# Kernel optimization log

Hardware: AMD Instinct MI355X
Metric: run time of the kernel (lower is better)

## Reference

```python
import jax, jax.numpy as jnp
import numpy as np

EMBED_SIZE = 2048
EBS = 512            # embed_block_size
NB = EMBED_SIZE // EBS  # num_blocks = 4
HEADS = 8
HD = EBS // HEADS    # head_dim = 64
N, S = 4, 1024


def block_linear(x, W, b):
    # x: [T, NB, EBS], W: [NB, EBS, EBS], b: [NB, EBS]
    return jnp.einsum('tbi,bio->tbo', x, W) + b


def setup_inputs() -> dict:
    key = jax.random.key(0)
    ks = jax.random.split(key, 11)
    sc = 1.0 / np.sqrt(EBS)
    inp = {
        'values': jax.random.normal(ks[0], (N, S, EMBED_SIZE), jnp.float32),
        'keys': jax.random.normal(ks[1], (N, S, EMBED_SIZE), jnp.float32),
        'query': jax.random.normal(ks[2], (N, S, EMBED_SIZE), jnp.float32),
        'mask': jnp.ones((N, 1, 1, S, S), jnp.int32),
        'Wv': jax.random.normal(ks[3], (NB, EBS, EBS), jnp.float32) * sc,
        'bv': jnp.zeros((NB, EBS), jnp.float32),
        'Wk': jax.random.normal(ks[4], (NB, EBS, EBS), jnp.float32) * sc,
        'bk': jnp.zeros((NB, EBS), jnp.float32),
        'Wq': jax.random.normal(ks[5], (NB, EBS, EBS), jnp.float32) * sc,
        'bq': jnp.zeros((NB, EBS), jnp.float32),
        'Wo': jax.random.normal(ks[6], (NB, EBS, EBS), jnp.float32) * sc,
        'bo': jnp.zeros((NB, EBS), jnp.float32),
    }
    return inp


def reference(values, keys, query, mask, Wv, bv, Wk, bk, Wq, bq, Wo, bo):
    n, ql = query.shape[0], query.shape[1]
    vl, kl = values.shape[1], keys.shape[1]
    # block-diagonal QKV projections
    v = block_linear(values.reshape(-1, NB, EBS), Wv, bv)
    k = block_linear(keys.reshape(-1, NB, EBS), Wk, bk)
    q = block_linear(query.reshape(-1, NB, EBS), Wq, bq)
    v = v.reshape(n, vl, NB, HEADS, HD)
    k = k.reshape(n, kl, NB, HEADS, HD)
    q = q.reshape(n, ql, NB, HEADS, HD)
    energy = jnp.einsum('nqbhd,nkbhd->nbhqk', q, k)
    energy = jnp.where(mask == 0, jnp.float32(-1e20), energy)
    # NOTE: faithful to original: softmax over dim=3 (the query axis of nbhqk)
    attention = jax.nn.softmax(energy / np.sqrt(HD), axis=3)
    out = jnp.einsum('nbhql,nlbhd->nqbhd', attention, v)
    out = out.reshape(n * ql, NB, HEADS * HD)
    out = block_linear(out, Wo, bo)
    return out.reshape(n, ql, -1)
```

## Files before the change

### kernel.cpp

```cpp
#include <hip/hip_runtime.h>


typedef unsigned short u16;
typedef __bf16 bf16x8 __attribute__((ext_vector_type(8)));
typedef float f32x4 __attribute__((ext_vector_type(4)));

#define S_LEN 1024
#define HD 64
#define EMB 2048
#define EBS 512
#define C2EXP 0.18033688011112042f

__device__ __forceinline__ u16 f2b(float f) {
    union { float f; unsigned int i; } x; x.f = f;
    return (u16)((x.i + 0x8000u) >> 16);
}
__device__ __forceinline__ float b2f(u16 u) {
    union { unsigned int i; float f; } x; x.i = ((unsigned int)u) << 16;
    return x.f;
}
__device__ __forceinline__ bf16x8 ld8(const u16* p) {
    return *reinterpret_cast<const bf16x8*>(p);
}
__device__ __forceinline__ unsigned int pack2(float a, float b) {
    union { float f; unsigned int i; } x, y; x.f = a; y.f = b;
    return ((x.i + 0x8000u) >> 16) | ((y.i + 0x8000u) & 0xFFFF0000u);
}
__device__ __forceinline__ int swz(int r, int c) {
    return (r << 6) + (c ^ ((r & 7) << 3));
}

__device__ __forceinline__ int dtype_probe(const void* src, int tid, int* s_flag) {
    if (tid < 64) {
        u16 v = ((const u16*)src)[tid * 2];
        int e = (v >> 7) & 0xFF;
        int sane = (e >= 117 && e <= 134);
        unsigned long long b = __ballot(sane);
        if (tid == 0) *s_flag = (__popcll(b) < 32) ? 1 : 0;
    }
    __syncthreads();
    return *s_flag;
}

__global__ __launch_bounds__(256) void wtrans(
    const void* __restrict__ Wv, const void* __restrict__ Wk,
    const void* __restrict__ Wq, const void* __restrict__ Wo,
    u16* __restrict__ WT, const void* __restrict__ probe)
{
    const int p = blockIdx.z >> 2, b = blockIdx.z & 3;
    const void* Wp = (p == 0 ? Wv : p == 1 ? Wk : p == 2 ? Wq : Wo);
    const size_t boff = (size_t)b * EBS * EBS;
    u16* D = WT + (size_t)(p * 4 + b) * EBS * EBS;
    const int i0 = blockIdx.x * 64, o0 = blockIdx.y * 64;
    const int tid = threadIdx.x;
    __shared__ __align__(16) u16 tile[64][72];
    __shared__ int s_flag;
    const int is32 = dtype_probe(probe, tid, &s_flag);
    for (int c = tid; c < 512; c += 256) {
        const int r = c >> 3, c8 = (c & 7) << 3;
        union { uint4 v; u16 u[8]; } pk;
        if (is32) {
            const float* src = (const float*)Wp + boff + (size_t)(i0 + r) * EBS + o0 + c8;
            const float4 f0 = *(const float4*)src, f1 = *(const float4*)(src + 4);
            pk.u[0] = f2b(f0.x); pk.u[1] = f2b(f0.y); pk.u[2] = f2b(f0.z); pk.u[3] = f2b(f0.w);
            pk.u[4] = f2b(f1.x); pk.u[5] = f2b(f1.y); pk.u[6] = f2b(f1.z); pk.u[7] = f2b(f1.w);
        } else {
            pk.v = *(const uint4*)((const u16*)Wp + boff + (size_t)(i0 + r) * EBS + o0 + c8);
        }
        *(uint4*)&tile[r][c8] = pk.v;
    }
    __syncthreads();
    for (int c = tid; c < 512; c += 256) {
        const int r = c >> 3, c8 = (c & 7) << 3;
        union { uint4 v; u16 u[8]; } pk;
        #pragma unroll
        for (int j = 0; j < 8; ++j) pk.u[j] = tile[c8 + j][r];
        *(uint4*)(D + (size_t)(o0 + r) * EBS + i0 + c8) = pk.v;
    }
}

__global__ __launch_bounds__(256) void gemm_qkv(
    const void* __restrict__ A, const void* __restrict__ W, const u16* __restrict__ WTp,
    const void* __restrict__ bias, u16* __restrict__ dst,
    const void* __restrict__ probe, int use_wt, int vmode, float oscale,
    const float* __restrict__ vsc)
{
    const int tm = blockIdx.x, tn = blockIdx.y, b = blockIdx.z;
    const int tid = threadIdx.x;
    const int wave = tid >> 6, lane = tid & 63, quad = lane >> 4, c16 = lane & 15;
    const int wm = wave >> 1, wn = wave & 1;

    __shared__ __align__(16) u16 Al[128 * 40];
    __shared__ __align__(16) u16 Bl[128 * 40];
    __shared__ int s_flag;
    const int is32 = dtype_probe(probe, tid, &s_flag);

    f32x4 acc[4][4];
    #pragma unroll
    for (int i = 0; i < 4; ++i)
        #pragma unroll
        for (int j = 0; j < 4; ++j) acc[i][j] = (f32x4){0.f, 0.f, 0.f, 0.f};

    const size_t aoff = (size_t)tm * 128 * EMB + (size_t)b * EBS;
    const u16*   Ab = (const u16*)A + aoff;
    const float* Af = (const float*)A + aoff;
    const size_t woff = (size_t)b * EBS * EBS + (size_t)tn * 128;
    const u16*   Wb = (const u16*)W + woff;
    const float* Wf = (const float*)W + woff;
    const u16*   Tb = WTp + (size_t)b * EBS * EBS + (size_t)tn * 128 * EBS;

    for (int k0 = 0; k0 < EBS; k0 += 32) {
        for (int c = tid; c < 512; c += 256) {
            const int r = c >> 2, c8 = (c & 3) << 3;
            if (is32) {
                const float* p = Af + (size_t)r * EMB + k0 + c8;
                const float4 f0 = *(const float4*)p, f1 = *(const float4*)(p + 4);
                union { uint4 v; u16 u[8]; } pk;
                pk.u[0] = f2b(f0.x); pk.u[1] = f2b(f0.y); pk.u[2] = f2b(f0.z); pk.u[3] = f2b(f0.w);
                pk.u[4] = f2b(f1.x); pk.u[5] = f2b(f1.y); pk.u[6] = f2b(f1.z); pk.u[7] = f2b(f1.w);
                *(uint4*)&Al[r * 40 + c8] = pk.v;
            } else {
                *(uint4*)&Al[r * 40 + c8] = *(const uint4*)(Ab + (size_t)r * EMB + k0 + c8);
            }
        }
        if (use_wt) {
            for (int c = tid; c < 512; c += 256) {
                const int r = c >> 2, c8 = (c & 3) << 3;
                *(uint4*)&Bl[r * 40 + c8] = *(const uint4*)(Tb + (size_t)r * EBS + k0 + c8);
            }
        } else {
            for (int c = tid; c < 512; c += 256) {
                const int i = c & 31, oc = c >> 5;
                u16 h[8];
                if (is32) {
                    const float* p = Wf + (size_t)(k0 + i) * EBS + oc * 8;
                    const float4 f0 = *(const float4*)p, f1 = *(const float4*)(p + 4);
                    h[0] = f2b(f0.x); h[1] = f2b(f0.y); h[2] = f2b(f0.z); h[3] = f2b(f0.w);
                    h[4] = f2b(f1.x); h[5] = f2b(f1.y); h[6] = f2b(f1.z); h[7] = f2b(f1.w);
                } else {
                    union { uint4 v; u16 u[8]; } pk;
                    pk.v = *(const uint4*)(Wb + (size_t)(k0 + i) * EBS + oc * 8);
                    #pragma unroll
                    for (int j = 0; j < 8; ++j) h[j] = pk.u[j];
                }
                #pragma unroll
                for (int j = 0; j < 8; ++j) Bl[(oc * 8 + j) * 40 + i] = h[j];
            }
        }
        __syncthreads();
        bf16x8 af[4], bfr[4];
        #pragma unroll
        for (int ms = 0; ms < 4; ++ms)
            af[ms] = ld8(&Al[(wm * 64 + ms * 16 + c16) * 40 + quad * 8]);
        #pragma unroll
        for (int ns = 0; ns < 4; ++ns)
            bfr[ns] = ld8(&Bl[(wn * 64 + ns * 16 + c16) * 40 + quad * 8]);
        if (vmode == 0) {
            #pragma unroll
            for (int ms = 0; ms < 4; ++ms)
                #pragma unroll
                for (int ns = 0; ns < 4; ++ns)
                    acc[ms][ns] = __builtin_amdgcn_mfma_f32_16x16x32_bf16(af[ms], bfr[ns], acc[ms][ns], 0, 0, 0);
        } else {
            #pragma unroll
            for (int ms = 0; ms < 4; ++ms)
                #pragma unroll
                for (int ns = 0; ns < 4; ++ns)
                    acc[ms][ns] = __builtin_amdgcn_mfma_f32_16x16x32_bf16(bfr[ns], af[ms], acc[ms][ns], 0, 0, 0);
        }
        __syncthreads();
    }

    if (vmode == 0) {
        #pragma unroll
        for (int ns = 0; ns < 4; ++ns) {
            const int o = tn * 128 + wn * 64 + ns * 16 + c16;
            const float bb = is32 ? ((const float*)bias)[b * EBS + o]
                                  : b2f(((const u16*)bias)[b * EBS + o]);
            #pragma unroll
            for (int ms = 0; ms < 4; ++ms) {
                #pragma unroll
                for (int r = 0; r < 4; ++r) {
                    const int t = tm * 128 + wm * 64 + ms * 16 + quad * 4 + r;
                    const int n = t >> 10, s = t & 1023;
                    const int h = o >> 6, d = o & 63;
                    const int hid = (n * 4 + b) * 8 + h;
                    dst[(size_t)hid * (S_LEN * HD) + (size_t)s * HD + d] = f2b((acc[ms][ns][r] + bb) * oscale);
                }
            }
        }
    } else {
        #pragma unroll
        for (int ns = 0; ns < 4; ++ns) {
            #pragma unroll
            for (int r = 0; r < 4; ++r) {
                const int o = tn * 128 + wn * 64 + ns * 16 + quad * 4 + r;
                const float bb = is32 ? ((const float*)bias)[b * EBS + o]
                                      : b2f(((const u16*)bias)[b * EBS + o]);
                const int h = o >> 6, d = o & 63;
                #pragma unroll
                for (int ms = 0; ms < 4; ++ms) {
                    const int t = tm * 128 + wm * 64 + ms * 16 + c16;
                    const int n = t >> 10, s = t & 1023;
                    const int hid = (n * 4 + b) * 8 + h;
                    float val = (acc[ms][ns][r] + bb) * oscale;
                    if (vsc) val *= vsc[(size_t)hid * S_LEN + s];
                    dst[(size_t)hid * (S_LEN * HD) + (size_t)d * S_LEN + s] = f2b(val);
                }
            }
        }
    }
}

__global__ __launch_bounds__(256) void attn_colstats(
    const u16* __restrict__ qws, const u16* __restrict__ kws,
    float* __restrict__ vscale)
{
    const int hid = blockIdx.x, lb = blockIdx.y;
    const int tid = threadIdx.x;
    const int wave = tid >> 6, lane = tid & 63, quad = lane >> 4, c16 = lane & 15;
    const int l0 = lb * 128;

    __shared__ __align__(16) u16 Ql[64 * 72];

    const u16* Kp = kws + (size_t)hid * (S_LEN * HD);
    const u16* Qp = qws + (size_t)hid * (S_LEN * HD);

    bf16x8 ak[2][2];
    #pragma unroll
    for (int s = 0; s < 2; ++s) {
        const size_t row = (size_t)(l0 + s * 64 + wave * 16 + c16) * HD;
        ak[s][0] = ld8(&Kp[row + quad * 8]);
        ak[s][1] = ld8(&Kp[row + 32 + quad * 8]);
    }

    float sum[2][4];
    #pragma unroll
    for (int s = 0; s < 2; ++s)
        #pragma unroll
        for (int r = 0; r < 4; ++r) sum[s][r] = 0.f;

    for (int q0 = 0; q0 < S_LEN; q0 += 64) {
        for (int c = tid; c < 512; c += 256) {
            const int r = c >> 3, c8 = (c & 7) << 3;
            *(uint4*)&Ql[r * 72 + c8] = *(const uint4*)(Qp + (size_t)(q0 + r) * HD + c8);
        }
        __syncthreads();
        #pragma unroll
        for (int qs = 0; qs < 4; ++qs) {
            const bf16x8 bq0 = ld8(&Ql[(qs * 16 + c16) * 72 + quad * 8]);
            const bf16x8 bq1 = ld8(&Ql[(qs * 16 + c16) * 72 + 32 + quad * 8]);
            #pragma unroll
            for (int s = 0; s < 2; ++s) {
                f32x4 e = (f32x4){0.f, 0.f, 0.f, 0.f};
                e = __builtin_amdgcn_mfma_f32_16x16x32_bf16(ak[s][0], bq0, e, 0, 0, 0);
                e = __builtin_amdgcn_mfma_f32_16x16x32_bf16(ak[s][1], bq1, e, 0, 0, 0);
                #pragma unroll
                for (int r = 0; r < 4; ++r)
                    sum[s][r] += exp2f(e[r]);
            }
        }
        __syncthreads();
    }
    #pragma unroll
    for (int s = 0; s < 2; ++s) {
        #pragma unroll
        for (int r = 0; r < 4; ++r) {
            float ss = sum[s][r];
            ss += __shfl_xor(ss, 1);
            ss += __shfl_xor(ss, 2);
            ss += __shfl_xor(ss, 4);
            ss += __shfl_xor(ss, 8);
            if (c16 == 0) {
                const int l = l0 + s * 64 + wave * 16 + quad * 4 + r;
                vscale[hid * S_LEN + l] = 1.0f / ss;
            }
        }
    }
}

__global__ __launch_bounds__(256) void attn_pass2(
    const u16* __restrict__ qws, const u16* __restrict__ kws, const u16* __restrict__ vws,
    u16* __restrict__ omid, float* __restrict__ dout, int out32)
{
    const int hid = blockIdx.x, qb = blockIdx.y;
    const int tid = threadIdx.x;
    const int wave = tid >> 6, lane = tid & 63, quad = lane >> 4, c16 = lane & 15;
    const int q0 = qb * 128;

    __shared__ __align__(16) u16 Kl[64 * 64];
    __shared__ __align__(16) u16 Vt[64 * 64];
    __shared__ __align__(16) u16 Pl[4][32 * 64];

    const u16* Qp  = qws + (size_t)hid * (S_LEN * HD);
    const u16* Kp  = kws + (size_t)hid * (S_LEN * HD);
    const u16* VpT = vws + (size_t)hid * (S_LEN * HD);
    u16* Pw = &Pl[wave][0];

    bf16x8 aq[2][2];
    #pragma unroll
    for (int s = 0; s < 2; ++s) {
        const size_t row = (size_t)(q0 + s * 64 + wave * 16 + c16) * HD;
        aq[s][0] = ld8(&Qp[row + quad * 8]);
        aq[s][1] = ld8(&Qp[row + 32 + quad * 8]);
    }

    f32x4 oacc[2][4];
    #pragma unroll
    for (int s = 0; s < 2; ++s)
        #pragma unroll
        for (int i = 0; i < 4; ++i) oacc[s][i] = (f32x4){0.f, 0.f, 0.f, 0.f};

    for (int l0 = 0; l0 < S_LEN; l0 += 64) {
        for (int c = tid; c < 512; c += 256) {
            const int r = c >> 3, c8 = (c & 7) << 3;
            *(uint4*)&Kl[swz(r, c8)] = *(const uint4*)(Kp + (size_t)(l0 + r) * HD + c8);
        }
        for (int c = tid; c < 512; c += 256) {
            const int r = c >> 3, c8 = (c & 7) << 3;
            *(uint4*)&Vt[swz(r, c8)] = *(const uint4*)(VpT + (size_t)r * S_LEN + l0 + c8);
        }
        __syncthreads();

        #pragma unroll
        for (int ls = 0; ls < 4; ++ls) {
            const int lr = ls * 16 + c16;
            const bf16x8 ak0 = ld8(&Kl[swz(lr, quad * 8)]);
            const bf16x8 ak1 = ld8(&Kl[swz(lr, 32 + quad * 8)]);
            #pragma unroll
            for (int s = 0; s < 2; ++s) {
                f32x4 e = (f32x4){0.f, 0.f, 0.f, 0.f};
                e = __builtin_amdgcn_mfma_f32_16x16x32_bf16(ak0, aq[s][0], e, 0, 0, 0);
                e = __builtin_amdgcn_mfma_f32_16x16x32_bf16(ak1, aq[s][1], e, 0, 0, 0);
                union { uint2 v; unsigned int w[2]; } pp;
                pp.w[0] = pack2(exp2f(e[0]), exp2f(e[1]));
                pp.w[1] = pack2(exp2f(e[2]), exp2f(e[3]));
                *(uint2*)&Pw[swz(s * 16 + c16, ls * 16 + quad * 4)] = pp.v;
            }
        }

        bf16x8 ap[2][2];
        #pragma unroll
        for (int s = 0; s < 2; ++s) {
            ap[s][0] = ld8(&Pw[swz(s * 16 + c16, quad * 8)]);
            ap[s][1] = ld8(&Pw[swz(s * 16 + c16, 32 + quad * 8)]);
        }
        #pragma unroll
        for (int ns = 0; ns < 4; ++ns) {
            const bf16x8 bv0 = ld8(&Vt[swz(ns * 16 + c16, quad * 8)]);
            const bf16x8 bv1 = ld8(&Vt[swz(ns * 16 + c16, 32 + quad * 8)]);
            #pragma unroll
            for (int s = 0; s < 2; ++s) {
                oacc[s][ns] = __builtin_amdgcn_mfma_f32_16x16x32_bf16(ap[s][0], bv0, oacc[s][ns], 0, 0, 0);
                oacc[s][ns] = __builtin_amdgcn_mfma_f32_16x16x32_bf16(ap[s][1], bv1, oacc[s][ns], 0, 0, 0);
            }
        }
        __syncthreads();
    }

    const int nn = hid >> 5, bb = (hid >> 3) & 3, hh = hid & 7;
    #pragma unroll
    for (int s = 0; s < 2; ++s) {
        #pragma unroll
        for (int ns = 0; ns < 4; ++ns) {
            #pragma unroll
            for (int r = 0; r < 4; ++r) {
                const int q = q0 + s * 64 + wave * 16 + quad * 4 + r;
                const int d = ns * 16 + c16;
                const size_t idx = (size_t)(nn * 1024 + q) * EMB + bb * EBS + hh * HD + d;
                if (out32) dout[idx] = oacc[s][ns][r];
                else       omid[idx] = f2b(oacc[s][ns][r]);
            }
        }
    }
}

__global__ __launch_bounds__(256) void gemm_final_wt(
    const u16* __restrict__ omid, const u16* __restrict__ WTo,
    const void* __restrict__ bias, float* __restrict__ C,
    const void* __restrict__ probe)
{
    const int tm = blockIdx.x, tn = blockIdx.y, b = blockIdx.z;
    const int tid = threadIdx.x;
    const int wave = tid >> 6, lane = tid & 63, quad = lane >> 4, c16 = lane & 15;
    const int wm = wave >> 1, wn = wave & 1;

    __shared__ __align__(16) u16 Al[128 * 40];
    __shared__ __align__(16) u16 Bl[128 * 40];
    __shared__ int s_flag;
    const int is32 = dtype_probe(probe, tid, &s_flag);

    f32x4 acc[4][4];
    #pragma unroll
    for (int i = 0; i < 4; ++i)
        #pragma unroll
        for (int j = 0; j < 4; ++j) acc[i][j] = (f32x4){0.f, 0.f, 0.f, 0.f};

    const u16* Ab = omid + (size_t)tm * 128 * EMB + (size_t)b * EBS;
    const u16* Tb = WTo + (size_t)b * EBS * EBS + (size_t)tn * 128 * EBS;

    for (int k0 = 0; k0 < EBS; k0 += 32) {
        for (int c = tid; c < 512; c += 256) {
            const int r = c >> 2, c8 = (c & 3) << 3;
            *(uint4*)&Al[r * 40 + c8] = *(const uint4*)(Ab + (size_t)r * EMB + k0 + c8);
        }
        for (int c = tid; c < 512; c += 256) {
            const int r = c >> 2, c8 = (c & 3) << 3;
            *(uint4*)&Bl[r * 40 + c8] = *(const uint4*)(Tb + (size_t)r * EBS + k0 + c8);
        }
        __syncthreads();
        bf16x8 af[4], bfr[4];
        #pragma unroll
        for (int ms = 0; ms < 4; ++ms)
            af[ms] = ld8(&Al[(wm * 64 + ms * 16 + c16) * 40 + quad * 8]);
        #pragma unroll
        for (int ns = 0; ns < 4; ++ns)
            bfr[ns] = ld8(&Bl[(wn * 64 + ns * 16 + c16) * 40 + quad * 8]);
        #pragma unroll
        for (int ms = 0; ms < 4; ++ms)
            #pragma unroll
            for (int ns = 0; ns < 4; ++ns)
                acc[ms][ns] = __builtin_amdgcn_mfma_f32_16x16x32_bf16(af[ms], bfr[ns], acc[ms][ns], 0, 0, 0);
        __syncthreads();
    }

    #pragma unroll
    for (int ns = 0; ns < 4; ++ns) {
        const int o = tn * 128 + wn * 64 + ns * 16 + c16;
        const float bb = is32 ? ((const float*)bias)[b * EBS + o]
                              : b2f(((const u16*)bias)[b * EBS + o]);
        #pragma unroll
        for (int ms = 0; ms < 4; ++ms) {
            #pragma unroll
            for (int r = 0; r < 4; ++r) {
                const int t = tm * 128 + wm * 64 + ms * 16 + quad * 4 + r;
                C[(size_t)t * EMB + (size_t)b * EBS + o] = acc[ms][ns][r] + bb;
            }
        }
    }
}

__global__ __launch_bounds__(1024) void gemm_final_inplace(
    float* __restrict__ C, const void* __restrict__ W, const void* __restrict__ bias,
    const void* __restrict__ probe)
{
    const int tm = blockIdx.x, b = blockIdx.y;
    const int tid = threadIdx.x;
    const int wave = tid >> 6, lane = tid & 63, quad = lane >> 4, c16 = lane & 15;
    const int wm = wave >> 3, wn = wave & 7;

    __shared__ __align__(16) u16 Al[128 * 40];
    __shared__ __align__(16) u16 Bl[512 * 40];
    __shared__ int s_flag;
    const int is32 = dtype_probe(probe, tid, &s_flag);

    f32x4 acc[4][4];
    #pragma unroll
    for (int i = 0; i < 4; ++i)
        #pragma unroll
        for (int j = 0; j < 4; ++j) acc[i][j] = (f32x4){0.f, 0.f, 0.f, 0.f};

    const float* Ab = C + (size_t)tm * 128 * EMB + (size_t)b * EBS;
    const u16*   Wb = (const u16*)W + (size_t)b * EBS * EBS;
    const float* Wf = (const float*)W + (size_t)b * EBS * EBS;

    for (int k0 = 0; k0 < EBS; k0 += 32) {
        for (int c = tid; c < 512; c += 1024) {
            const int r = c >> 2, c8 = (c & 3) << 3;
            const float* p = Ab + (size_t)r * EMB + k0 + c8;
            const float4 f0 = *(const float4*)p, f1 = *(const float4*)(p + 4);
            union { uint4 v; u16 u[8]; } pk;
            pk.u[0] = f2b(f0.x); pk.u[1] = f2b(f0.y); pk.u[2] = f2b(f0.z); pk.u[3] = f2b(f0.w);
            pk.u[4] = f2b(f1.x); pk.u[5] = f2b(f1.y); pk.u[6] = f2b(f1.z); pk.u[7] = f2b(f1.w);
            *(uint4*)&Al[r * 40 + c8] = pk.v;
        }
        for (int c = tid; c < 2048; c += 1024) {
            const int i = c & 31, oc = c >> 5;
            u16 h[8];
            if (is32) {
                const float* p = Wf + (size_t)(k0 + i) * EBS + oc * 8;
                const float4 f0 = *(const float4*)p, f1 = *(const float4*)(p + 4);
                h[0] = f2b(f0.x); h[1] = f2b(f0.y); h[2] = f2b(f0.z); h[3] = f2b(f0.w);
                h[4] = f2b(f1.x); h[5] = f2b(f1.y); h[6] = f2b(f1.z); h[7] = f2b(f1.w);
            } else {
                union { uint4 v; u16 u[8]; } pk;
                pk.v = *(const uint4*)(Wb + (size_t)(k0 + i) * EBS + oc * 8);
                #pragma unroll
                for (int j = 0; j < 8; ++j) h[j] = pk.u[j];
            }
            #pragma unroll
            for (int j = 0; j < 8; ++j) Bl[(oc * 8 + j) * 40 + i] = h[j];
        }
        __syncthreads();
        bf16x8 af[4], bfr[4];
        #pragma unroll
        for (int ms = 0; ms < 4; ++ms)
            af[ms] = ld8(&Al[(wm * 64 + ms * 16 + c16) * 40 + quad * 8]);
        #pragma unroll
        for (int ns = 0; ns < 4; ++ns)
            bfr[ns] = ld8(&Bl[(wn * 64 + ns * 16 + c16) * 40 + quad * 8]);
        #pragma unroll
        for (int ms = 0; ms < 4; ++ms)
            #pragma unroll
            for (int ns = 0; ns < 4; ++ns)
                acc[ms][ns] = __builtin_amdgcn_mfma_f32_16x16x32_bf16(af[ms], bfr[ns], acc[ms][ns], 0, 0, 0);
        __syncthreads();
    }

    #pragma unroll
    for (int ns = 0; ns < 4; ++ns) {
        const int o = wn * 64 + ns * 16 + c16;
        const float bb = is32 ? ((const float*)bias)[b * EBS + o]
                              : b2f(((const u16*)bias)[b * EBS + o]);
        #pragma unroll
        for (int ms = 0; ms < 4; ++ms) {
            #pragma unroll
            for (int r = 0; r < 4; ++r) {
                const int t = tm * 128 + wm * 64 + ms * 16 + quad * 4 + r;
                C[(size_t)t * EMB + (size_t)b * EBS + o] = acc[ms][ns][r] + bb;
            }
        }
    }
}

extern "C" void kernel_launch(void* const* d_in, const int* in_sizes, int n_in,
                              void* d_out, int out_size, void* d_ws, size_t ws_size,
                              hipStream_t stream)
{
    (void)in_sizes; (void)n_in; (void)out_size;

    const void* values = d_in[0];
    const void* keys   = d_in[1];
    const void* query  = d_in[2];
    const void* Wv = d_in[4];  const void* bv = d_in[5];
    const void* Wk = d_in[6];  const void* bk = d_in[7];
    const void* Wq = d_in[8];  const void* bq = d_in[9];
    const void* Wo = d_in[10]; const void* bo = d_in[11];

    char* ws = (char*)d_ws;
    u16* qws = (u16*)(ws);
    u16* kws = (u16*)(ws + (16ull << 20));
    u16* vws = (u16*)(ws + (32ull << 20));
    float* out = (float*)d_out;

    const bool full = ws_size >= (73ull << 20);

    if (full) {
        u16* omid  = (u16*)(ws + (48ull << 20));
        u16* WT    = (u16*)(ws + (64ull << 20));
        float* vscale = (float*)(ws + (72ull << 20));
        u16* WTv = WT;
        u16* WTk = WT + (1u << 20);
        u16* WTq = WT + (2u << 20);
        u16* WTo = WT + (3u << 20);

        wtrans<<<dim3(8, 8, 16), 256, 0, stream>>>(Wv, Wk, Wq, Wo, WT, values);
        gemm_qkv<<<dim3(32, 4, 4), 256, 0, stream>>>(keys,   Wk, WTk, bk, kws, values, 1, 0, 1.0f, nullptr);
        gemm_qkv<<<dim3(32, 4, 4), 256, 0, stream>>>(query,  Wq, WTq, bq, qws, values, 1, 0, C2EXP, nullptr);
        attn_colstats<<<dim3(128, 8), 256, 0, stream>>>(qws, kws, vscale);
        gemm_qkv<<<dim3(32, 4, 4), 256, 0, stream>>>(values, Wv, WTv, bv, vws, values, 1, 1, 1.0f, vscale);
        attn_pass2<<<dim3(128, 8), 256, 0, stream>>>(qws, kws, vws, omid, out, 0);
        gemm_final_wt<<<dim3(32, 4, 4), 256, 0, stream>>>(omid, WTo, bo, out, values);
    } else {
        float* vscale = (float*)(ws + (48ull << 20));
        gemm_qkv<<<dim3(32, 4, 4), 256, 0, stream>>>(keys,   Wk, (const u16*)Wk, bk, kws, values, 0, 0, 1.0f, nullptr);
        gemm_qkv<<<dim3(32, 4, 4), 256, 0, stream>>>(query,  Wq, (const u16*)Wq, bq, qws, values, 0, 0, C2EXP, nullptr);
        attn_colstats<<<dim3(128, 8), 256, 0, stream>>>(qws, kws, vscale);
        gemm_qkv<<<dim3(32, 4, 4), 256, 0, stream>>>(values, Wv, (const u16*)Wv, bv, vws, values, 0, 1, 1.0f, vscale);
        attn_pass2<<<dim3(128, 8), 256, 0, stream>>>(qws, kws, vws, (u16*)out, out, 1);
        gemm_final_inplace<<<dim3(32, 4), 1024, 0, stream>>>(out, Wo, bo, values);
    }
}
```

Before: 423.3 us.

## Pre-convert inputs to bf16, async double-buffered LDS loads in GEMMs and attention

Adds a conversion kernel that turns the fp32 keys, query and values into bf16 up front. A new GEMM kernel uses global_load_lds double buffering with a swizzled layout and MFMA priority hints, and it replaces both the QKV and the output projections. The column-stats and attention kernels also switch to async double-buffered tile loads, and attention grows to 512 threads covering 256 queries per block. The aim is to hide global-load latency and remove fp32 conversion from the GEMM inner loops, at the cost of extra conversion passes that read and write the full activations in memory.

After: 357.4 us. -15.6%, faster.

```diff
diff --git a/kernel.cpp b/kernel.cpp
--- a/kernel.cpp
+++ b/kernel.cpp
@@ -3,6 +3,7 @@
 
 typedef unsigned short u16;
 typedef __bf16 bf16x8 __attribute__((ext_vector_type(8)));
+typedef __bf16 bf16x2 __attribute__((ext_vector_type(2)));
 typedef float f32x4 __attribute__((ext_vector_type(4)));
 
 #define S_LEN 1024
@@ -22,12 +23,13 @@
 __device__ __forceinline__ bf16x8 ld8(const u16* p) {
     return *reinterpret_cast<const bf16x8*>(p);
 }
-__device__ __forceinline__ unsigned int pack2(float a, float b) {
-    union { float f; unsigned int i; } x, y; x.f = a; y.f = b;
-    return ((x.i + 0x8000u) >> 16) | ((y.i + 0x8000u) & 0xFFFF0000u);
-}
 __device__ __forceinline__ int swz(int r, int c) {
     return (r << 6) + (c ^ ((r & 7) << 3));
+}
+__device__ __forceinline__ void gload16(const u16* g, u16* l) {
+    __builtin_amdgcn_global_load_lds(
+        (const __attribute__((address_space(1))) void*)g,
+        (__attribute__((address_space(3))) void*)l, 16, 0, 0);
 }
 
 __device__ __forceinline__ int dtype_probe(const void* src, int tid, int* s_flag) {
@@ -79,6 +81,161 @@
     }
 }
 
+__global__ __launch_bounds__(256) void conv_bf(
+    const void* __restrict__ s0, u16* __restrict__ d0,
+    const void* __restrict__ s1, u16* __restrict__ d1)
+{
+    const int which = blockIdx.y;
+    const void* s = which ? s1 : s0;
+    u16* d = which ? d1 : d0;
+    __shared__ int s_flag;
+    const int is32 = dtype_probe(s, threadIdx.x, &s_flag);
+    const int N8 = (4 * 1024 * 2048) / 8;
+    const int stride = gridDim.x * 256;
+    for (int i = blockIdx.x * 256 + threadIdx.x; i < N8; i += stride) {
+        if (is32) {
+            const float* p = (const float*)s + (size_t)i * 8;
+            const float4 f0 = *(const float4*)p, f1 = *(const float4*)(p + 4);
+            union { uint4 v; u16 u[8]; } pk;
+            pk.u[0] = f2b(f0.x); pk.u[1] = f2b(f0.y); pk.u[2] = f2b(f0.z); pk.u[3] = f2b(f0.w);
+            pk.u[4] = f2b(f1.x); pk.u[5] = f2b(f1.y); pk.u[6] = f2b(f1.z); pk.u[7] = f2b(f1.w);
+            *(uint4*)(d + (size_t)i * 8) = pk.v;
+        } else {
+            *(uint4*)(d + (size_t)i * 8) = ((const uint4*)s)[i];
+        }
+    }
+}
+
+__global__ __launch_bounds__(256) void gemm_fast(
+    const u16* __restrict__ Abf, const u16* __restrict__ WTp,
+    const void* __restrict__ bias, u16* __restrict__ dst, float* __restrict__ Cf,
+    const void* __restrict__ probe, int vmode, float oscale,
+    const float* __restrict__ vsc)
+{
+    const int tm = blockIdx.x, tn = blockIdx.y, b = blockIdx.z;
+    const int tid = threadIdx.x;
+    const int wave = tid >> 6, lane = tid & 63, quad = lane >> 4, c16 = lane & 15;
+    const int wm = wave >> 1, wn = wave & 1;
+
+    __shared__ __align__(16) u16 Al[2][128 * 32];
+    __shared__ __align__(16) u16 Bl[2][128 * 32];
+    __shared__ int s_flag;
+    const int is32 = dtype_probe(probe, tid, &s_flag);
+
+    f32x4 acc[4][4];
+    #pragma unroll
+    for (int i = 0; i < 4; ++i)
+        #pragma unroll
+        for (int j = 0; j < 4; ++j) acc[i][j] = (f32x4){0.f, 0.f, 0.f, 0.f};
+
+    const int rl = lane >> 2;
+    const int scol = (((lane & 3) ^ (rl & 3)) << 3);
+    const u16* aSrc0 = Abf + (size_t)(tm * 128 + wave * 32 + rl) * EMB + (size_t)b * EBS + scol;
+    const u16* aSrc1 = aSrc0 + (size_t)16 * EMB;
+    const u16* Tb = WTp + (size_t)b * EBS * EBS + (size_t)tn * 128 * EBS;
+    const u16* bSrc0 = Tb + (size_t)(wave * 32 + rl) * EBS + scol;
+    const u16* bSrc1 = bSrc0 + (size_t)16 * EBS;
+    u16* aDst0 = &Al[0][0] + wave * 1024;
+    u16* aDst1 = aDst0 + 512;
+    u16* bDst0 = &Bl[0][0] + wave * 1024;
+    u16* bDst1 = bDst0 + 512;
+
+    gload16(aSrc0, aDst0); gload16(aSrc1, aDst1);
+    gload16(bSrc0, bDst0); gload16(bSrc1, bDst1);
+    __syncthreads();
+
+    const int offA = (quad * 8) ^ ((c16 & 3) << 3);
+    int cur = 0;
+    for (int k0 = 0; k0 < EBS; k0 += 32) {
+        if (k0 + 32 < EBS) {
+            const int kn = k0 + 32, bo = (cur ^ 1) * 4096;
+            gload16(aSrc0 + kn, aDst0 + bo); gload16(aSrc1 + kn, aDst1 + bo);
+            gload16(bSrc0 + kn, bDst0 + bo); gload16(bSrc1 + kn, bDst1 + bo);
+        }
+        const u16* Ab = &Al[cur][0];
+        const u16* Bb = &Bl[cur][0];
+        bf16x8 af[4], bfr[4];
+        #pragma unroll
+        for (int ms = 0; ms < 4; ++ms)
+            af[ms] = ld8(&Ab[(wm * 64 + ms * 16 + c16) * 32 + offA]);
+        #pragma unroll
+        for (int ns = 0; ns < 4; ++ns)
+            bfr[ns] = ld8(&Bb[(wn * 64 + ns * 16 + c16) * 32 + offA]);
+        __builtin_amdgcn_s_setprio(1);
+        if (vmode == 0) {
+            #pragma unroll
+            for (int ms = 0; ms < 4; ++ms)
+                #pragma unroll
+                for (int ns = 0; ns < 4; ++ns)
+                    acc[ms][ns] = __builtin_amdgcn_mfma_f32_16x16x32_bf16(af[ms], bfr[ns], acc[ms][ns], 0, 0, 0);
+        } else {
+            #pragma unroll
+            for (int ms = 0; ms < 4; ++ms)
+                #pragma unroll
+                for (int ns = 0; ns < 4; ++ns)
+                    acc[ms][ns] = __builtin_amdgcn_mfma_f32_16x16x32_bf16(bfr[ns], af[ms], acc[ms][ns], 0, 0, 0);
+        }
+        __builtin_amdgcn_s_setprio(0);
+        __syncthreads();
+        cur ^= 1;
+    }
+
+    if (Cf) {
+        #pragma unroll
+        for (int ns = 0; ns < 4; ++ns) {
+            const int o = tn * 128 + wn * 64 + ns * 16 + c16;
+            const float bb = is32 ? ((const float*)bias)[b * EBS + o]
+                                  : b2f(((const u16*)bias)[b * EBS + o]);
+            #pragma unroll
+            for (int ms = 0; ms < 4; ++ms) {
+                #pragma unroll
+                for (int r = 0; r < 4; ++r) {
+                    const int t = tm * 128 + wm * 64 + ms * 16 + quad * 4 + r;
+                    Cf[(size_t)t * EMB + (size_t)b * EBS + o] = acc[ms][ns][r] + bb;
+                }
+            }
+        }
+    } else if (vmode == 0) {
+        #pragma unroll
+        for (int ns = 0; ns < 4; ++ns) {
+            const int o = tn * 128 + wn * 64 + ns * 16 + c16;
+            const float bb = is32 ? ((const float*)bias)[b * EBS + o]
+                                  : b2f(((const u16*)bias)[b * EBS + o]);
+            #pragma unroll
+            for (int ms = 0; ms < 4; ++ms) {
+                #pragma unroll
+                for (int r = 0; r < 4; ++r) {
+                    const int t = tm * 128 + wm * 64 + ms * 16 + quad * 4 + r;
+                    const int n = t >> 10, s = t & 1023;
+                    const int h = o >> 6, d = o & 63;
+                    const int hid = (n * 4 + b) * 8 + h;
+                    dst[(size_t)hid * (S_LEN * HD) + (size_t)s * HD + d] = f2b((acc[ms][ns][r] + bb) * oscale);
+                }
+            }
+        }
+    } else {
+        #pragma unroll
+        for (int ns = 0; ns < 4; ++ns) {
+            #pragma unroll
+            for (int r = 0; r < 4; ++r) {
+                const int o = tn * 128 + wn * 64 + ns * 16 + quad * 4 + r;
+                const float bb = is32 ? ((const float*)bias)[b * EBS + o]
+                                      : b2f(((const u16*)bias)[b * EBS + o]);
+                const int h = o >> 6, d = o & 63;
+                #pragma unroll
+                for (int ms = 0; ms < 4; ++ms) {
+                    const int t = tm * 128 + wm * 64 + ms * 16 + c16;
+                    const int n = t >> 10, s = t & 1023;
+                    const int hid = (n * 4 + b) * 8 + h;
+                    float val = (acc[ms][ns][r] + bb) * oscale;
+                    if (vsc) val *= vsc[(size_t)hid * S_LEN + s];
+                    dst[(size_t)hid * (S_LEN * HD) + (size_t)d * S_LEN + s] = f2b(val);
+                }
+            }
+        }
+    }
+}
+
 __global__ __launch_bounds__(256) void gemm_qkv(
     const void* __restrict__ A, const void* __restrict__ W, const u16* __restrict__ WTp,
     const void* __restrict__ bias, u16* __restrict__ dst,
@@ -221,7 +378,7 @@
     const int wave = tid >> 6, lane = tid & 63, quad = lane >> 4, c16 = lane & 15;
     const int l0 = lb * 128;
 
-    __shared__ __align__(16) u16 Ql[64 * 72];
+    __shared__ __align__(16) u16 Ql[2][64 * 64];
 
     const u16* Kp = kws + (size_t)hid * (S_LEN * HD);
     const u16* Qp = qws + (size_t)hid * (S_LEN * HD);
@@ -240,27 +397,43 @@
         #pragma unroll
         for (int r = 0; r < 4; ++r) sum[s][r] = 0.f;
 
-    for (int q0 = 0; q0 < S_LEN; q0 += 64) {
-        for (int c = tid; c < 512; c += 256) {
-            const int r = c >> 3, c8 = (c & 7) << 3;
-            *(uint4*)&Ql[r * 72 + c8] = *(const uint4*)(Qp + (size_t)(q0 + r) * HD + c8);
-        }
-        __syncthreads();
+    const int srow = lane >> 3;
+    const int scol = (((lane & 7) ^ srow) << 3);
+    const u16* qSrc0 = Qp + (size_t)(wave * 16 + srow) * HD + scol;
+    const u16* qSrc1 = qSrc0 + (size_t)8 * HD;
+    u16* qDst0 = &Ql[0][0] + wave * 1024;
+    u16* qDst1 = qDst0 + 512;
+
+    gload16(qSrc0, qDst0); gload16(qSrc1, qDst1);
+    __syncthreads();
+
+    int cur = 0;
+    for (int t = 0; t < 16; ++t) {
+        if (t < 15) {
+            const size_t off = (size_t)(t + 1) * 64 * HD;
+            const int bo = (cur ^ 1) * 4096;
+            gload16(qSrc0 + off, qDst0 + bo);
+            gload16(qSrc1 + off, qDst1 + bo);
+        }
+        const u16* Qb = &Ql[cur][0];
         #pragma unroll
         for (int qs = 0; qs < 4; ++qs) {
-            const bf16x8 bq0 = ld8(&Ql[(qs * 16 + c16) * 72 + quad * 8]);
-            const bf16x8 bq1 = ld8(&Ql[(qs * 16 + c16) * 72 + 32 + quad * 8]);
+            const bf16x8 bq0 = ld8(&Qb[swz(qs * 16 + c16, quad * 8)]);
+            const bf16x8 bq1 = ld8(&Qb[swz(qs * 16 + c16, 32 + quad * 8)]);
             #pragma unroll
             for (int s = 0; s < 2; ++s) {
                 f32x4 e = (f32x4){0.f, 0.f, 0.f, 0.f};
+                __builtin_amdgcn_s_setprio(1);
                 e = __builtin_amdgcn_mfma_f32_16x16x32_bf16(ak[s][0], bq0, e, 0, 0, 0);
                 e = __builtin_amdgcn_mfma_f32_16x16x32_bf16(ak[s][1], bq1, e, 0, 0, 0);
+                __builtin_amdgcn_s_setprio(0);
                 #pragma unroll
                 for (int r = 0; r < 4; ++r)
                     sum[s][r] += exp2f(e[r]);
             }
         }
         __syncthreads();
+        cur ^= 1;
     }
     #pragma unroll
     for (int s = 0; s < 2; ++s) {
@@ -279,18 +452,18 @@
     }
 }
 
-__global__ __launch_bounds__(256) void attn_pass2(
+__global__ __launch_bounds__(512) void attn_pass2(
     const u16* __restrict__ qws, const u16* __restrict__ kws, const u16* __restrict__ vws,
     u16* __restrict__ omid, float* __restrict__ dout, int out32)
 {
     const int hid = blockIdx.x, qb = blockIdx.y;
     const int tid = threadIdx.x;
     const int wave = tid >> 6, lane = tid & 63, quad = lane >> 4, c16 = lane & 15;
-    const int q0 = qb * 128;
-
-    __shared__ __align__(16) u16 Kl[64 * 64];
-    __shared__ __align__(16) u16 Vt[64 * 64];
-    __shared__ __align__(16) u16 Pl[4][32 * 64];
+    const int q0 = qb * 256;
+
+    __shared__ __align__(16) u16 Kl[2][64 * 64];
+    __shared__ __align__(16) u16 Vt[2][64 * 64];
+    __shared__ __align__(16) u16 Pl[8][32 * 64];
 
     const u16* Qp  = qws + (size_t)hid * (S_LEN * HD);
     const u16* Kp  = kws + (size_t)hid * (S_LEN * HD);
@@ -300,7 +473,7 @@
     bf16x8 aq[2][2];
     #pragma unroll
     for (int s = 0; s < 2; ++s) {
-        const size_t row = (size_t)(q0 + s * 64 + wave * 16 + c16) * HD;
+        const size_t row = (size_t)(q0 + s * 128 + wave * 16 + c16) * HD;
         aq[s][0] = ld8(&Qp[row + quad * 8]);
         aq[s][1] = ld8(&Qp[row + 32 + quad * 8]);
     }
@@ -311,30 +484,43 @@
         #pragma unroll
         for (int i = 0; i < 4; ++i) oacc[s][i] = (f32x4){0.f, 0.f, 0.f, 0.f};
 
-    for (int l0 = 0; l0 < S_LEN; l0 += 64) {
-        for (int c = tid; c < 512; c += 256) {
-            const int r = c >> 3, c8 = (c & 7) << 3;
-            *(uint4*)&Kl[swz(r, c8)] = *(const uint4*)(Kp + (size_t)(l0 + r) * HD + c8);
-        }
-        for (int c = tid; c < 512; c += 256) {
-            const int r = c >> 3, c8 = (c & 7) << 3;
-            *(uint4*)&Vt[swz(r, c8)] = *(const uint4*)(VpT + (size_t)r * S_LEN + l0 + c8);
-        }
-        __syncthreads();
+    const int srow = lane >> 3;
+    const int scol = (((lane & 7) ^ srow) << 3);
+    const u16* kSrc = Kp + (size_t)(wave * 8 + srow) * HD + scol;
+    const u16* vSrc = VpT + (size_t)(wave * 8 + srow) * S_LEN + scol;
+    u16* kDst = &Kl[0][0] + wave * 512;
+    u16* vDst = &Vt[0][0] + wave * 512;
+
+    gload16(kSrc, kDst);
+    gload16(vSrc, vDst);
+    __syncthreads();
+
+    int cur = 0;
+    for (int t = 0; t < 16; ++t) {
+        if (t < 15) {
+            const int l0n = (t + 1) * 64;
+            const int bo = (cur ^ 1) * 4096;
+            gload16(kSrc + (size_t)l0n * HD, kDst + bo);
+            gload16(vSrc + l0n, vDst + bo);
+        }
+        const u16* Kb = &Kl[cur][0];
+        const u16* Vb = &Vt[cur][0];
 
         #pragma unroll
         for (int ls = 0; ls < 4; ++ls) {
             const int lr = ls * 16 + c16;
-            const bf16x8 ak0 = ld8(&Kl[swz(lr, quad * 8)]);
-            const bf16x8 ak1 = ld8(&Kl[swz(lr, 32 + quad * 8)]);
+            const bf16x8 ak0 = ld8(&Kb[swz(lr, quad * 8)]);
+            const bf16x8 ak1 = ld8(&Kb[swz(lr, 32 + quad * 8)]);
             #pragma unroll
             for (int s = 0; s < 2; ++s) {
                 f32x4 e = (f32x4){0.f, 0.f, 0.f, 0.f};
+                __builtin_amdgcn_s_setprio(1);
                 e = __builtin_amdgcn_mfma_f32_16x16x32_bf16(ak0, aq[s][0], e, 0, 0, 0);
                 e = __builtin_amdgcn_mfma_f32_16x16x32_bf16(ak1, aq[s][1], e, 0, 0, 0);
-                union { uint2 v; unsigned int w[2]; } pp;
-                pp.w[0] = pack2(exp2f(e[0]), exp2f(e[1]));
-                pp.w[1] = pack2(exp2f(e[2]), exp2f(e[3]));
+                __builtin_amdgcn_s_setprio(0);
+                union { uint2 v; bf16x2 h[2]; } pp;
+                pp.h[0] = (bf16x2){(__bf16)exp2f(e[0]), (__bf16)exp2f(e[1])};
+                pp.h[1] = (bf16x2){(__bf16)exp2f(e[2]), (__bf16)exp2f(e[3])};
                 *(uint2*)&Pw[swz(s * 16 + c16, ls * 16 + quad * 4)] = pp.v;
             }
         }
@@ -345,17 +531,20 @@
             ap[s][0] = ld8(&Pw[swz(s * 16 + c16, quad * 8)]);
             ap[s][1] = ld8(&Pw[swz(s * 16 + c16, 32 + quad * 8)]);
         }
+        __builtin_amdgcn_s_setprio(1);
         #pragma unroll
         for (int ns = 0; ns < 4; ++ns) {
-            const bf16x8 bv0 = ld8(&Vt[swz(ns * 16 + c16, quad * 8)]);
-            const bf16x8 bv1 = ld8(&Vt[swz(ns * 16 + c16, 32 + quad * 8)]);
+            const bf16x8 bv0 = ld8(&Vb[swz(ns * 16 + c16, quad * 8)]);
+            const bf16x8 bv1 = ld8(&Vb[swz(ns * 16 + c16, 32 + quad * 8)]);
             #pragma unroll
             for (int s = 0; s < 2; ++s) {
                 oacc[s][ns] = __builtin_amdgcn_mfma_f32_16x16x32_bf16(ap[s][0], bv0, oacc[s][ns], 0, 0, 0);
                 oacc[s][ns] = __builtin_amdgcn_mfma_f32_16x16x32_bf16(ap[s][1], bv1, oacc[s][ns], 0, 0, 0);
             }
         }
+        __builtin_amdgcn_s_setprio(0);
         __syncthreads();
+        cur ^= 1;
     }
 
     const int nn = hid >> 5, bb = (hid >> 3) & 3, hh = hid & 7;
@@ -365,76 +554,11 @@
         for (int ns = 0; ns < 4; ++ns) {
             #pragma unroll
             for (int r = 0; r < 4; ++r) {
-                const int q = q0 + s * 64 + wave * 16 + quad * 4 + r;
+                const int q = q0 + s * 128 + wave * 16 + quad * 4 + r;
                 const int d = ns * 16 + c16;
                 const size_t idx = (size_t)(nn * 1024 + q) * EMB + bb * EBS + hh * HD + d;
                 if (out32) dout[idx] = oacc[s][ns][r];
                 else       omid[idx] = f2b(oacc[s][ns][r]);
-            }
-        }
-    }
-}
-
-__global__ __launch_bounds__(256) void gemm_final_wt(
-    const u16* __restrict__ omid, const u16* __restrict__ WTo,
-    const void* __restrict__ bias, float* __restrict__ C,
-    const void* __restrict__ probe)
-{
-    const int tm = blockIdx.x, tn = blockIdx.y, b = blockIdx.z;
-    const int tid = threadIdx.x;
-    const int wave = tid >> 6, lane = tid & 63, quad = lane >> 4, c16 = lane & 15;
-    const int wm = wave >> 1, wn = wave & 1;
-
-    __shared__ __align__(16) u16 Al[128 * 40];
-    __shared__ __align__(16) u16 Bl[128 * 40];
-    __shared__ int s_flag;
-    const int is32 = dtype_probe(probe, tid, &s_flag);
-
-    f32x4 acc[4][4];
-    #pragma unroll
-    for (int i = 0; i < 4; ++i)
-        #pragma unroll
-        for (int j = 0; j < 4; ++j) acc[i][j] = (f32x4){0.f, 0.f, 0.f, 0.f};
-
-    const u16* Ab = omid + (size_t)tm * 128 * EMB + (size_t)b * EBS;
-    const u16* Tb = WTo + (size_t)b * EBS * EBS + (size_t)tn * 128 * EBS;
-
-    for (int k0 = 0; k0 < EBS; k0 += 32) {
-        for (int c = tid; c < 512; c += 256) {
-            const int r = c >> 2, c8 = (c & 3) << 3;
-            *(uint4*)&Al[r * 40 + c8] = *(const uint4*)(Ab + (size_t)r * EMB + k0 + c8);
-        }
-        for (int c = tid; c < 512; c += 256) {
-            const int r = c >> 2, c8 = (c & 3) << 3;
-            *(uint4*)&Bl[r * 40 + c8] = *(const uint4*)(Tb + (size_t)r * EBS + k0 + c8);
-        }
-        __syncthreads();
-        bf16x8 af[4], bfr[4];
-        #pragma unroll
-        for (int ms = 0; ms < 4; ++ms)
-            af[ms] = ld8(&Al[(wm * 64 + ms * 16 + c16) * 40 + quad * 8]);
-        #pragma unroll
-        for (int ns = 0; ns < 4; ++ns)
-            bfr[ns] = ld8(&Bl[(wn * 64 + ns * 16 + c16) * 40 + quad * 8]);
-        #pragma unroll
-        for (int ms = 0; ms < 4; ++ms)
-            #pragma unroll
-            for (int ns = 0; ns < 4; ++ns)
-                acc[ms][ns] = __builtin_amdgcn_mfma_f32_16x16x32_bf16(af[ms], bfr[ns], acc[ms][ns], 0, 0, 0);
-        __syncthreads();
-    }
-
-    #pragma unroll
-    for (int ns = 0; ns < 4; ++ns) {
-        const int o = tn * 128 + wn * 64 + ns * 16 + c16;
-        const float bb = is32 ? ((const float*)bias)[b * EBS + o]
-                              : b2f(((const u16*)bias)[b * EBS + o]);
-        #pragma unroll
-        for (int ms = 0; ms < 4; ++ms) {
-            #pragma unroll
-            for (int r = 0; r < 4; ++r) {
-                const int t = tm * 128 + wm * 64 + ms * 16 + quad * 4 + r;
-                C[(size_t)t * EMB + (size_t)b * EBS + o] = acc[ms][ns][r] + bb;
             }
         }
     }
@@ -553,21 +677,26 @@
         u16* WTk = WT + (1u << 20);
         u16* WTq = WT + (2u << 20);
         u16* WTo = WT + (3u << 20);
+        u16* kbf = vws;
+        u16* qbf = omid;
+        u16* vbf = omid;
 
         wtrans<<<dim3(8, 8, 16), 256, 0, stream>>>(Wv, Wk, Wq, Wo, WT, values);
-        gemm_qkv<<<dim3(32, 4, 4), 256, 0, stream>>>(keys,   Wk, WTk, bk, kws, values, 1, 0, 1.0f, nullptr);
-        gemm_qkv<<<dim3(32, 4, 4), 256, 0, stream>>>(query,  Wq, WTq, bq, qws, values, 1, 0, C2EXP, nullptr);
+        conv_bf<<<dim3(1024, 2), 256, 0, stream>>>(keys, kbf, query, qbf);
+        gemm_fast<<<dim3(32, 4, 4), 256, 0, stream>>>(kbf, WTk, bk, kws, nullptr, values, 0, 1.0f, nullptr);
+        gemm_fast<<<dim3(32, 4, 4), 256, 0, stream>>>(qbf, WTq, bq, qws, nullptr, values, 0, C2EXP, nullptr);
+        conv_bf<<<dim3(1024, 1), 256, 0, stream>>>(values, vbf, values, vbf);
         attn_colstats<<<dim3(128, 8), 256, 0, stream>>>(qws, kws, vscale);
-        gemm_qkv<<<dim3(32, 4, 4), 256, 0, stream>>>(values, Wv, WTv, bv, vws, values, 1, 1, 1.0f, vscale);
-        attn_pass2<<<dim3(128, 8), 256, 0, stream>>>(qws, kws, vws, omid, out, 0);
-        gemm_final_wt<<<dim3(32, 4, 4), 256, 0, stream>>>(omid, WTo, bo, out, values);
+        gemm_fast<<<dim3(32, 4, 4), 256, 0, stream>>>(vbf, WTv, bv, vws, nullptr, values, 1, 1.0f, vscale);
+        attn_pass2<<<dim3(128, 4), 512, 0, stream>>>(qws, kws, vws, omid, out, 0);
+        gemm_fast<<<dim3(32, 4, 4), 256, 0, stream>>>(omid, WTo, bo, nullptr, out, values, 0, 1.0f, nullptr);
     } else {
         float* vscale = (float*)(ws + (48ull << 20));
         gemm_qkv<<<dim3(32, 4, 4), 256, 0, stream>>>(keys,   Wk, (const u16*)Wk, bk, kws, values, 0, 0, 1.0f, nullptr);
         gemm_qkv<<<dim3(32, 4, 4), 256, 0, stream>>>(query,  Wq, (const u16*)Wq, bq, qws, values, 0, 0, C2EXP, nullptr);
         attn_colstats<<<dim3(128, 8), 256, 0, stream>>>(qws, kws, vscale);
         gemm_qkv<<<dim3(32, 4, 4), 256, 0, stream>>>(values, Wv, (const u16*)Wv, bv, vws, values, 0, 1, 1.0f, vscale);
-        attn_pass2<<<dim3(128, 8), 256, 0, stream>>>(qws, kws, vws, (u16*)out, out, 1);
+        attn_pass2<<<dim3(128, 4), 512, 0, stream>>>(qws, kws, vws, (u16*)out, out, 1);
         gemm_final_inplace<<<dim3(32, 4), 1024, 0, stream>>>(out, Wo, bo, values);
     }
 }
```
